# Optimization experiments

Hardware: AMD Instinct MI355X
Metric: run time of the kernel (lower is better)

The kernel has to match this reference:

```python
import jax, jax.numpy as jnp
import numpy as np

N_HEAD = 16
D_MODEL = 1024
D_HEAD = 64
SCALE = 1.0 / D_HEAD ** 0.5
LN_EPS = 1e-5


def layer_norm(x, g, b):
    mu = jnp.mean(x, axis=-1, keepdims=True)
    var = jnp.mean(jnp.square(x - mu), axis=-1, keepdims=True)
    return (x - mu) * jax.lax.rsqrt(var + LN_EPS) * g + b


def setup_inputs() -> dict:
    key = jax.random.key(0)
    ks = jax.random.split(key, 6)
    T, B = 2048, 4
    h = jax.random.normal(ks[0], (T, B, D_MODEL), dtype=jnp.float32)
    # key-padding mask, shape (klen, bsz); True = masked
    attn_mask = jax.random.randint(ks[1], (T, B), 0, 2).astype(jnp.bool_)
    s = 1.0 / np.sqrt(D_MODEL)
    wq = jax.random.uniform(ks[2], (N_HEAD * D_HEAD, D_MODEL), minval=-s, maxval=s, dtype=jnp.float32)
    wkv = jax.random.uniform(ks[3], (2 * N_HEAD * D_HEAD, D_MODEL), minval=-s, maxval=s, dtype=jnp.float32)
    wo = jax.random.uniform(ks[4], (D_MODEL, N_HEAD * D_HEAD), minval=-s, maxval=s, dtype=jnp.float32)
    ln_g = jnp.ones((D_MODEL,), jnp.float32)
    ln_b = jnp.zeros((D_MODEL,), jnp.float32)
    return {"h": h, "attn_mask": attn_mask, "wq": wq, "wkv": wkv,
            "wo": wo, "ln_g": ln_g, "ln_b": ln_b}


def reference(h, attn_mask, wq, wkv, wo, ln_g, ln_b):
    T, B, _ = h.shape
    c = h  # mems is None
    head_q = (h @ wq.T).reshape(T, B, N_HEAD, D_HEAD)
    kv = c @ wkv.T
    head_k, head_v = jnp.split(kv, 2, axis=-1)
    head_k = head_k.reshape(T, B, N_HEAD, D_HEAD)
    head_v = head_v.reshape(T, B, N_HEAD, D_HEAD)

    # scores: [qlen, klen, bsz, n_head]
    attn_score = jnp.einsum('ibnd,jbnd->ijbn', head_q, head_k) * SCALE
    attn_score = jnp.where(attn_mask[None, :, :, None], -jnp.inf, attn_score)
    attn_prob = jax.nn.softmax(attn_score, axis=1)

    attn_vec = jnp.einsum('ijbn,jbnd->ibnd', attn_prob, head_v)
    attn_vec = attn_vec.reshape(T, B, N_HEAD * D_HEAD)
    attn_out = attn_vec @ wo.T
    # post-lnorm residual (pre_lnorm=False); gate='plus' path unused here
    return layer_norm(h + attn_out, ln_g, ln_b)
```

## Files before the change

kernel.cpp:

```cpp
#include <hip/hip_runtime.h>

#define T_LEN 2048
#define BSZ 4
#define NHEAD 16
#define DHEAD 64
#define DMODEL 1024
#define SCALE 0.125f
#define L2E_SCALE (0.125f * 1.44269504f)
#define ROW 72

typedef __bf16 bf16x8 __attribute__((ext_vector_type(8)));
typedef float f32x4 __attribute__((ext_vector_type(4)));

__device__ __forceinline__ float bf2f(unsigned short u) {
  union { unsigned int i; float f; } v; v.i = ((unsigned int)u) << 16; return v.f;
}
__device__ __forceinline__ unsigned short f2bf(float f) {
  union { float f; unsigned int i; } v; v.f = f;
  unsigned int r = v.i + 0x7fffu + ((v.i >> 16) & 1u);
  return (unsigned short)(r >> 16);
}

typedef __attribute__((address_space(1))) void* gptr_t;
typedef __attribute__((address_space(3))) void* lptr_t;

__device__ __forceinline__ void load_lds16(const void* g, void* l) {
  __builtin_amdgcn_global_load_lds((gptr_t)g, (lptr_t)l, 16, 0, 0);
}

__global__ __launch_bounds__(256) void cvt_prep(const float* __restrict__ h,
                                                const float* __restrict__ wq,
                                                const float* __restrict__ wkv,
                                                const float* __restrict__ wo,
                                                const unsigned char* __restrict__ mask,
                                                unsigned short* __restrict__ h_bf,
                                                unsigned short* __restrict__ wq_bf,
                                                unsigned short* __restrict__ wkv_bf,
                                                unsigned short* __restrict__ wo_bf,
                                                int* __restrict__ pos,
                                                int* __restrict__ nkeys) {
  const int tid = threadIdx.x;
  if (blockIdx.x < 12288) {
    const size_t E4 = (size_t)T_LEN * BSZ * DMODEL / 4;
    const size_t W4 = (size_t)NHEAD * DHEAD * DMODEL / 4;
    const size_t g = (size_t)blockIdx.x * 256 + tid;
    const float* src; unsigned short* dst; size_t off;
    if (g < E4)                { src = h;   dst = h_bf;   off = g; }
    else if (g < E4 + W4)      { src = wq;  dst = wq_bf;  off = g - E4; }
    else if (g < E4 + 3 * W4)  { src = wkv; dst = wkv_bf; off = g - E4 - W4; }
    else                       { src = wo;  dst = wo_bf;  off = g - E4 - 3 * W4; }
    const float4 v = *(const float4*)(src + off * 4);
    ushort4 o;
    o.x = f2bf(v.x); o.y = f2bf(v.y); o.z = f2bf(v.z); o.w = f2bf(v.w);
    *(ushort4*)(dst + off * 4) = o;
    return;
  }
  __shared__ int s_any;
  if (tid == 0) s_any = 0;
  __syncthreads();
  int acc = 0;
  for (int i = tid; i < T_LEN * BSZ; i += 256)
    if ((i & 3) != 0 && mask[i] != 0) acc = 1;
  if (acc) atomicOr(&s_any, 1);
  __syncthreads();
  const int mmode = s_any ? 0 : 1;
  const int wv = tid >> 6, lane = tid & 63;
  const int b = wv;
  int run = 0;
  for (int j0 = 0; j0 < T_LEN; j0 += 64) {
    const int j = j0 + lane;
    const int mval = mmode ? ((const int*)mask)[(size_t)j * BSZ + b]
                           : (int)mask[(size_t)j * BSZ + b];
    const int keep = (mval == 0) ? 1 : 0;
    int x = keep;
#pragma unroll
    for (int off = 1; off < 64; off <<= 1) {
      const int y = __shfl_up(x, off, 64);
      if (lane >= off) x += y;
    }
    pos[b * T_LEN + j] = keep ? (run + x - keep) : -1;
    run += __shfl(x, 63, 64);
  }
  if (lane == 0) nkeys[b] = run;
}

#define GEMM64_DBUF(Aptr, Bptr)                                                        \
  const int tid  = threadIdx.x;                                                        \
  const int lane = tid & 63;                                                           \
  const int wv   = tid >> 6;                                                           \
  const int wr = (wv >> 1) * 64;                                                       \
  const int wc = (wv & 1) * 64;                                                        \
  const int mi   = lane & 15;                                                          \
  const int quad = lane >> 4;                                                          \
  f32x4 acc[4][4] = {};                                                                \
  int rowc[4], colc[4];                                                                \
  _Pragma("unroll")                                                                    \
  for (int c = 0; c < 4; c++) {                                                        \
    const int s = c * 256 + tid;                                                       \
    rowc[c] = s >> 3;                                                                  \
    colc[c] = ((s & 7) ^ (rowc[c] & 7)) * 8;                                           \
  }                                                                                    \
  const int swz = mi & 7;                                                              \
  _Pragma("unroll")                                                                    \
  for (int c = 0; c < 4; c++) {                                                        \
    load_lds16(Aptr + (size_t)rowc[c] * DMODEL + colc[c], As + c * 2048 + wv * 512);   \
    load_lds16(Bptr + (size_t)rowc[c] * DMODEL + colc[c], Bs + c * 2048 + wv * 512);   \
  }                                                                                    \
  for (int k0 = 0; k0 < DMODEL; k0 += 64) {                                            \
    const int cur = (k0 >> 6) & 1;                                                     \
    const unsigned short* Asr = As + cur * 8192;                                       \
    const unsigned short* Bsr = Bs + cur * 8192;                                       \
    unsigned short* Asw = As + (1 - cur) * 8192;                                       \
    unsigned short* Bsw = Bs + (1 - cur) * 8192;                                       \
    __syncthreads();                                                                   \
    if (k0 + 64 < DMODEL) {                                                            \
      _Pragma("unroll")                                                                \
      for (int c = 0; c < 4; c++) {                                                    \
        load_lds16(Aptr + (size_t)rowc[c] * DMODEL + k0 + 64 + colc[c], Asw + c * 2048 + wv * 512); \
        load_lds16(Bptr + (size_t)rowc[c] * DMODEL + k0 + 64 + colc[c], Bsw + c * 2048 + wv * 512); \
      }                                                                                \
    }                                                                                  \
    _Pragma("unroll")                                                                  \
    for (int kq = 0; kq < 2; kq++) {                                                   \
      const int cp = ((kq * 4 + quad) ^ swz) * 8;                                      \
      bf16x8 af[4], bfr[4];                                                            \
      _Pragma("unroll")                                                                \
      for (int rt = 0; rt < 4; rt++)                                                   \
        af[rt] = *(const bf16x8*)(Asr + (wr + rt * 16 + mi) * 64 + cp);                \
      _Pragma("unroll")                                                                \
      for (int ct = 0; ct < 4; ct++)                                                   \
        bfr[ct] = *(const bf16x8*)(Bsr + (wc + ct * 16 + mi) * 64 + cp);               \
      _Pragma("unroll")                                                                \
      for (int rt = 0; rt < 4; rt++)                                                   \
        _Pragma("unroll")                                                              \
        for (int ct = 0; ct < 4; ct++)                                                 \
          acc[rt][ct] = __builtin_amdgcn_mfma_f32_16x16x32_bf16(af[rt], bfr[ct], acc[rt][ct], 0, 0, 0); \
    }                                                                                  \
  }

__global__ __launch_bounds__(256) void gemm_qkv(const unsigned short* __restrict__ A,
                                                const unsigned short* __restrict__ Wq,
                                                const unsigned short* __restrict__ Wkv,
                                                const int* __restrict__ pos,
                                                unsigned short* __restrict__ outQ,
                                                unsigned short* __restrict__ outK,
                                                unsigned short* __restrict__ outVt) {
  __shared__ alignas(16) unsigned short As[2 * 128 * 64];
  __shared__ alignas(16) unsigned short Bs[2 * 128 * 64];
  const int m0 = blockIdx.y * 128;
  const int n0 = blockIdx.x * 128;
  const unsigned short* Abase = A + (size_t)m0 * DMODEL;
  const unsigned short* Bbase = (n0 < DMODEL) ? (Wq + (size_t)n0 * DMODEL)
                                              : (Wkv + (size_t)(n0 - DMODEL) * DMODEL);
  GEMM64_DBUF(Abase, Bbase)

  const int region = n0 >> 10;
#pragma unroll
  for (int rt = 0; rt < 4; rt++) {
#pragma unroll
    for (int r = 0; r < 4; r++) {
      const int gm = m0 + wr + rt * 16 + quad * 4 + r;
      const int i = gm >> 2, b = gm & 3;
      int p = i;
      if (region > 0) p = pos[b * T_LEN + i];
      if (region > 0 && p < 0) continue;
#pragma unroll
      for (int ct = 0; ct < 4; ct++) {
        const int gn = n0 + wc + ct * 16 + mi;
        const int gnl = gn & (DMODEL - 1);
        const int hn = gnl >> 6, d = gnl & 63;
        const float v = acc[rt][ct][r];
        if (region == 0)
          outQ[(((size_t)b * NHEAD + hn) * T_LEN + i) * DHEAD + d] = f2bf(v * L2E_SCALE);
        else if (region == 1)
          outK[(((size_t)b * NHEAD + hn) * T_LEN + p) * DHEAD + d] = f2bf(v);
        else
          outVt[(((size_t)b * NHEAD + hn) * DHEAD + d) * T_LEN + p] = f2bf(v);
      }
    }
  }
}

__global__ __launch_bounds__(256) void gemm_out(const unsigned short* __restrict__ A,
                                                const unsigned short* __restrict__ Bw,
                                                unsigned short* __restrict__ outB) {
  __shared__ alignas(16) unsigned short As[2 * 128 * 64];
  __shared__ alignas(16) unsigned short Bs[2 * 128 * 64];
  const int m0 = blockIdx.y * 128;
  const int n0 = blockIdx.x * 128;
  const unsigned short* Abase = A  + (size_t)m0 * DMODEL;
  const unsigned short* Bbase = Bw + (size_t)n0 * DMODEL;
  GEMM64_DBUF(Abase, Bbase)

#pragma unroll
  for (int rt = 0; rt < 4; rt++)
#pragma unroll
    for (int ct = 0; ct < 4; ct++)
#pragma unroll
      for (int r = 0; r < 4; r++) {
        const int gm = m0 + wr + rt * 16 + quad * 4 + r;
        const int gn = n0 + wc + ct * 16 + mi;
        outB[(size_t)gm * DMODEL + gn] = f2bf(acc[rt][ct][r]);
      }
}

template<bool TAIL>
__device__ __forceinline__ void attn_chunk(int j0, int nk, int mi, int quad,
    const unsigned short* Ks, const unsigned short* Vts, unsigned short* PsW,
    const bf16x8 (&qb)[2][2], f32x4 (&oc)[2][4], float (&rs)[2]) {
  f32x4 sc[2][4] = {};
#pragma unroll
  for (int ct = 0; ct < 4; ct++) {
    const bf16x8 kf0 = *(const bf16x8*)(Ks + (ct * 16 + mi) * ROW + quad * 8);
    const bf16x8 kf1 = *(const bf16x8*)(Ks + (ct * 16 + mi) * ROW + 32 + quad * 8);
#pragma unroll
    for (int g = 0; g < 2; g++) {
      sc[g][ct] = __builtin_amdgcn_mfma_f32_16x16x32_bf16(kf0, qb[g][0], sc[g][ct], 0, 0, 0);
      sc[g][ct] = __builtin_amdgcn_mfma_f32_16x16x32_bf16(kf1, qb[g][1], sc[g][ct], 0, 0, 0);
    }
  }
#pragma unroll
  for (int g = 0; g < 2; g++)
#pragma unroll
    for (int ct = 0; ct < 4; ct++) {
#pragma unroll
      for (int r = 0; r < 4; r++) {
        float p = __builtin_amdgcn_exp2f(sc[g][ct][r]);
        if (TAIL && (j0 + ct * 16 + quad * 4 + r >= nk)) p = 0.f;
        rs[g] += p;
        sc[g][ct][r] = p;
      }
      union { float f; unsigned u; } c0, c1, c2, c3;
      c0.f = sc[g][ct][0]; c1.f = sc[g][ct][1]; c2.f = sc[g][ct][2]; c3.f = sc[g][ct][3];
      const unsigned pk0 = (c0.u >> 16) | (c1.u & 0xFFFF0000u);
      const unsigned pk1 = (c2.u >> 16) | (c3.u & 0xFFFF0000u);
      *(uint2*)(PsW + (g * 16 + mi) * ROW + ct * 16 + quad * 4) = make_uint2(pk0, pk1);
    }
  bf16x8 pa0[2], pa1[2];
#pragma unroll
  for (int g = 0; g < 2; g++) {
    pa0[g] = *(const bf16x8*)(PsW + (g * 16 + mi) * ROW + quad * 8);
    pa1[g] = *(const bf16x8*)(PsW + (g * 16 + mi) * ROW + 32 + quad * 8);
  }
#pragma unroll
  for (int ct = 0; ct < 4; ct++) {
    const bf16x8 vf0 = *(const bf16x8*)(Vts + (ct * 16 + mi) * ROW + quad * 8);
    const bf16x8 vf1 = *(const bf16x8*)(Vts + (ct * 16 + mi) * ROW + 32 + quad * 8);
#pragma unroll
    for (int g = 0; g < 2; g++) {
      oc[g][ct] = __builtin_amdgcn_mfma_f32_16x16x32_bf16(pa0[g], vf0, oc[g][ct], 0, 0, 0);
      oc[g][ct] = __builtin_amdgcn_mfma_f32_16x16x32_bf16(pa1[g], vf1, oc[g][ct], 0, 0, 0);
    }
  }
}

__global__ __launch_bounds__(256, 4) void attn_mfma(const unsigned short* __restrict__ Qg,
                                                    const unsigned short* __restrict__ Kg,
                                                    const unsigned short* __restrict__ Vtg,
                                                    const int* __restrict__ nkeys,
                                                    unsigned short* __restrict__ av) {
  __shared__ alignas(16) unsigned short smem[18688];
  unsigned short* Ks  = smem;
  unsigned short* Vts = smem + 4608;
  unsigned short* Qs  = smem + 9216;
  float* Ls = (float*)(smem + 18432);

  const int tid  = threadIdx.x;
  const int lane = tid & 63;
  const int wv   = tid >> 6;
  const int mi   = lane & 15;
  const int quad = lane >> 4;
  const int i0 = blockIdx.x * 128;
  const int b  = blockIdx.y;
  const int n  = blockIdx.z;
  const size_t base = ((size_t)b * NHEAD + n) * T_LEN * DHEAD;
  const int nk = nkeys[b];

  for (int it = tid; it < 1024; it += 256) {
    const int r = it >> 3, c8 = (it & 7) * 8;
    *(uint4*)(Qs + r * ROW + c8) = *(const uint4*)(Qg + base + (size_t)(i0 + r) * DHEAD + c8);
  }
  __syncthreads();
  bf16x8 qb[2][2];
#pragma unroll
  for (int g = 0; g < 2; g++) {
    qb[g][0] = *(const bf16x8*)(Qs + (wv * 32 + g * 16 + mi) * ROW + quad * 8);
    qb[g][1] = *(const bf16x8*)(Qs + (wv * 32 + g * 16 + mi) * ROW + 32 + quad * 8);
  }

  f32x4 oc[2][4] = {};
  float rs[2] = {0.f, 0.f};
  unsigned short* PsW = Qs + wv * 2304;

  const int nmain = nk & ~63;
  for (int j0 = 0; j0 < nmain; j0 += 64) {
    for (int it = tid; it < 512; it += 256) {
      const int r = it >> 3, c8 = (it & 7) * 8;
      *(uint4*)(Ks  + r * ROW + c8) = *(const uint4*)(Kg  + base + (size_t)(j0 + r) * DHEAD + c8);
      *(uint4*)(Vts + r * ROW + c8) = *(const uint4*)(Vtg + base + (size_t)r * T_LEN + j0 + c8);
    }
    __syncthreads();
    attn_chunk<false>(j0, nk, mi, quad, Ks, Vts, PsW, qb, oc, rs);
    __syncthreads();
  }
  if (nmain < nk) {
    for (int it = tid; it < 512; it += 256) {
      const int r = it >> 3, c8 = (it & 7) * 8;
      *(uint4*)(Ks  + r * ROW + c8) = *(const uint4*)(Kg  + base + (size_t)(nmain + r) * DHEAD + c8);
      *(uint4*)(Vts + r * ROW + c8) = *(const uint4*)(Vtg + base + (size_t)r * T_LEN + nmain + c8);
    }
    __syncthreads();
    attn_chunk<true>(nmain, nk, mi, quad, Ks, Vts, PsW, qb, oc, rs);
  }

#pragma unroll
  for (int g = 0; g < 2; g++) {
    float t = rs[g];
    t += __shfl_xor(t, 16, 64);
    t += __shfl_xor(t, 32, 64);
    rs[g] = t;
  }
  if (quad == 0) { Ls[wv * 32 + mi] = rs[0]; Ls[wv * 32 + 16 + mi] = rs[1]; }
  __syncthreads();
  float linv[2][4];
#pragma unroll
  for (int g = 0; g < 2; g++)
#pragma unroll
    for (int r = 0; r < 4; r++) {
      const float l = Ls[wv * 32 + g * 16 + quad * 4 + r];
      linv[g][r] = (l > 0.f) ? (1.f / l) : 0.f;
    }
#pragma unroll
  for (int g = 0; g < 2; g++)
#pragma unroll
    for (int ct = 0; ct < 4; ct++)
#pragma unroll
      for (int r = 0; r < 4; r++) {
        const int q = i0 + wv * 32 + g * 16 + quad * 4 + r;
        const int d = ct * 16 + mi;
        av[((size_t)q * BSZ + b) * DMODEL + n * DHEAD + d] = f2bf(oc[g][ct][r] * linv[g][r]);
      }
}

__global__ __launch_bounds__(256) void ln_kernel(const float* __restrict__ h,
                                                 const unsigned short* __restrict__ ao,
                                                 const float* __restrict__ g,
                                                 const float* __restrict__ bb,
                                                 float* __restrict__ out) {
  __shared__ float red[16];
  const int row = blockIdx.x;
  const int tid = threadIdx.x;
  const size_t base = (size_t)row * DMODEL;
  const int c = tid * 4;
  const float4 hv = *(const float4*)(h + base + c);
  const ushort4 a4 = *(const ushort4*)(ao + base + c);
  float x[4] = { hv.x + bf2f(a4.x), hv.y + bf2f(a4.y), hv.z + bf2f(a4.z), hv.w + bf2f(a4.w) };
  float s = 0.f, sq = 0.f;
#pragma unroll
  for (int k = 0; k < 4; k++) { s += x[k]; sq += x[k] * x[k]; }
#pragma unroll
  for (int off = 32; off; off >>= 1) { s += __shfl_xor(s, off, 64); sq += __shfl_xor(sq, off, 64); }
  const int wv = tid >> 6, lane = tid & 63;
  if (lane == 0) { red[wv] = s; red[8 + wv] = sq; }
  __syncthreads();
  if (tid == 0) {
    float ts = 0.f, tq = 0.f;
    for (int w = 0; w < 4; w++) { ts += red[w]; tq += red[8 + w]; }
    red[4] = ts; red[12] = tq;
  }
  __syncthreads();
  const float mu  = red[4] * (1.f / DMODEL);
  const float var = red[12] * (1.f / DMODEL) - mu * mu;
  const float inv = rsqrtf(var + 1e-5f);
  const float4 gv = *(const float4*)(g + c);
  const float4 bv = *(const float4*)(bb + c);
  float4 o;
  o.x = (x[0] - mu) * inv * gv.x + bv.x;
  o.y = (x[1] - mu) * inv * gv.y + bv.y;
  o.z = (x[2] - mu) * inv * gv.z + bv.z;
  o.w = (x[3] - mu) * inv * gv.w + bv.w;
  *(float4*)(out + base + c) = o;
}

extern "C" void kernel_launch(void* const* d_in, const int* in_sizes, int n_in,
                              void* d_out, int out_size, void* d_ws, size_t ws_size,
                              hipStream_t stream) {
  (void)in_sizes; (void)n_in; (void)out_size; (void)ws_size;
  const float* h           = (const float*)d_in[0];
  const unsigned char* msk = (const unsigned char*)d_in[1];
  const float* wq          = (const float*)d_in[2];
  const float* wkv         = (const float*)d_in[3];
  const float* wo          = (const float*)d_in[4];
  const float* lng         = (const float*)d_in[5];
  const float* lnb         = (const float*)d_in[6];
  float* out = (float*)d_out;

  const size_t E  = (size_t)T_LEN * BSZ * DMODEL;
  const size_t WQ = (size_t)NHEAD * DHEAD * DMODEL;
  char* ws = (char*)d_ws;
  int* nkeys            = (int*)ws;                       ws += 16;
  int* pos              = (int*)ws;                       ws += (size_t)BSZ * T_LEN * 4;
  unsigned short* h_bf  = (unsigned short*)ws;            ws += E * 2;
  unsigned short* wq_bf = (unsigned short*)ws;            ws += WQ * 2;
  unsigned short* wkv_bf= (unsigned short*)ws;            ws += 2 * WQ * 2;
  unsigned short* wo_bf = (unsigned short*)ws;            ws += WQ * 2;
  unsigned short* Qb    = (unsigned short*)ws;            ws += E * 2;
  unsigned short* Kb    = (unsigned short*)ws;            ws += E * 2;
  unsigned short* Vtb   = (unsigned short*)ws;            ws += E * 2;
  unsigned short* AV    = (unsigned short*)ws;            ws += E * 2;
  unsigned short* AO    = (unsigned short*)ws;

  const dim3 blk(256);
  cvt_prep<<<dim3(12289), blk, 0, stream>>>(h, wq, wkv, wo, msk,
                                            h_bf, wq_bf, wkv_bf, wo_bf, pos, nkeys);
  gemm_qkv<<<dim3(3 * DMODEL / 128, T_LEN * BSZ / 128), blk, 0, stream>>>(
      h_bf, wq_bf, wkv_bf, pos, Qb, Kb, Vtb);
  attn_mfma<<<dim3(T_LEN / 128, BSZ, NHEAD), blk, 0, stream>>>(Qb, Kb, Vtb, nkeys, AV);
  gemm_out<<<dim3(DMODEL / 128, T_LEN * BSZ / 128), blk, 0, stream>>>(AV, wo_bf, AO);
  ln_kernel<<<dim3(T_LEN * BSZ), blk, 0, stream>>>(h, AO, lng, lnb, out);
}
```

Before: 312.7 us.

## Rewrite QKV and output GEMMs with larger tiles and a 4-stage LDS ring

```diff
diff --git a/kernel.cpp b/kernel.cpp
--- a/kernel.cpp
+++ b/kernel.cpp
@@ -84,92 +84,133 @@
   if (lane == 0) nkeys[b] = run;
 }
 
-#define GEMM64_DBUF(Aptr, Bptr)                                                        \
-  const int tid  = threadIdx.x;                                                        \
-  const int lane = tid & 63;                                                           \
-  const int wv   = tid >> 6;                                                           \
-  const int wr = (wv >> 1) * 64;                                                       \
-  const int wc = (wv & 1) * 64;                                                        \
-  const int mi   = lane & 15;                                                          \
-  const int quad = lane >> 4;                                                          \
-  f32x4 acc[4][4] = {};                                                                \
-  int rowc[4], colc[4];                                                                \
-  _Pragma("unroll")                                                                    \
-  for (int c = 0; c < 4; c++) {                                                        \
-    const int s = c * 256 + tid;                                                       \
-    rowc[c] = s >> 3;                                                                  \
-    colc[c] = ((s & 7) ^ (rowc[c] & 7)) * 8;                                           \
-  }                                                                                    \
-  const int swz = mi & 7;                                                              \
-  _Pragma("unroll")                                                                    \
-  for (int c = 0; c < 4; c++) {                                                        \
-    load_lds16(Aptr + (size_t)rowc[c] * DMODEL + colc[c], As + c * 2048 + wv * 512);   \
-    load_lds16(Bptr + (size_t)rowc[c] * DMODEL + colc[c], Bs + c * 2048 + wv * 512);   \
-  }                                                                                    \
-  for (int k0 = 0; k0 < DMODEL; k0 += 64) {                                            \
-    const int cur = (k0 >> 6) & 1;                                                     \
-    const unsigned short* Asr = As + cur * 8192;                                       \
-    const unsigned short* Bsr = Bs + cur * 8192;                                       \
-    unsigned short* Asw = As + (1 - cur) * 8192;                                       \
-    unsigned short* Bsw = Bs + (1 - cur) * 8192;                                       \
-    __syncthreads();                                                                   \
-    if (k0 + 64 < DMODEL) {                                                            \
-      _Pragma("unroll")                                                                \
-      for (int c = 0; c < 4; c++) {                                                    \
-        load_lds16(Aptr + (size_t)rowc[c] * DMODEL + k0 + 64 + colc[c], Asw + c * 2048 + wv * 512); \
-        load_lds16(Bptr + (size_t)rowc[c] * DMODEL + k0 + 64 + colc[c], Bsw + c * 2048 + wv * 512); \
-      }                                                                                \
-    }                                                                                  \
-    _Pragma("unroll")                                                                  \
-    for (int kq = 0; kq < 2; kq++) {                                                   \
-      const int cp = ((kq * 4 + quad) ^ swz) * 8;                                      \
-      bf16x8 af[4], bfr[4];                                                            \
-      _Pragma("unroll")                                                                \
-      for (int rt = 0; rt < 4; rt++)                                                   \
-        af[rt] = *(const bf16x8*)(Asr + (wr + rt * 16 + mi) * 64 + cp);                \
-      _Pragma("unroll")                                                                \
-      for (int ct = 0; ct < 4; ct++)                                                   \
-        bfr[ct] = *(const bf16x8*)(Bsr + (wc + ct * 16 + mi) * 64 + cp);               \
-      _Pragma("unroll")                                                                \
-      for (int rt = 0; rt < 4; rt++)                                                   \
-        _Pragma("unroll")                                                              \
-        for (int ct = 0; ct < 4; ct++)                                                 \
-          acc[rt][ct] = __builtin_amdgcn_mfma_f32_16x16x32_bf16(af[rt], bfr[ct], acc[rt][ct], 0, 0, 0); \
-    }                                                                                  \
-  }
-
-__global__ __launch_bounds__(256) void gemm_qkv(const unsigned short* __restrict__ A,
-                                                const unsigned short* __restrict__ Wq,
-                                                const unsigned short* __restrict__ Wkv,
-                                                const int* __restrict__ pos,
-                                                unsigned short* __restrict__ outQ,
-                                                unsigned short* __restrict__ outK,
-                                                unsigned short* __restrict__ outVt) {
-  __shared__ alignas(16) unsigned short As[2 * 128 * 64];
-  __shared__ alignas(16) unsigned short Bs[2 * 128 * 64];
-  const int m0 = blockIdx.y * 128;
-  const int n0 = blockIdx.x * 128;
+
+__device__ __forceinline__ bf16x8 ldfrag(const unsigned short* slot, int row, int quad) {
+  return *(const bf16x8*)(slot + row * 32 + (((quad ^ (row >> 1)) & 3) * 8));
+}
+
+template<int C>
+__device__ __forceinline__ void stage32(const unsigned short* gsrc,
+                                        unsigned short* slot, int tid) {
+#pragma unroll
+  for (int c = 0; c < C; ++c) {
+    const int g = c * 512 + tid;
+    const int row = g >> 2;
+    const int lc = (g ^ (row >> 1)) & 3;
+    load_lds16(gsrc + (size_t)row * DMODEL + lc * 8,
+               slot + c * 4096 + (tid >> 6) * 512);
+  }
+}
+
+template<int N>
+__device__ __forceinline__ void wait_vm() {
+  if constexpr (N == 0)      asm volatile("s_waitcnt vmcnt(0)" ::: "memory");
+  else if constexpr (N == 3) asm volatile("s_waitcnt vmcnt(3)" ::: "memory");
+  else if constexpr (N == 4) asm volatile("s_waitcnt vmcnt(4)" ::: "memory");
+  else if constexpr (N == 6) asm volatile("s_waitcnt vmcnt(6)" ::: "memory");
+  else                       asm volatile("s_waitcnt vmcnt(8)" ::: "memory");
+}
+
+template<int MF, int NF, int BRA, int BRB>
+__device__ __forceinline__ void gemm_ring(const unsigned short* __restrict__ Abase,
+                                          const unsigned short* __restrict__ Bbase,
+                                          unsigned short* As, unsigned short* Bs,
+                                          f32x4 (&acc)[MF][NF],
+                                          int tid, int mi, int quad, int wrow, int wcol) {
+  constexpr int LA = BRA / 128, LB = BRB / 128;
+  constexpr int SA = BRA * 32, SB = BRB * 32;
+  constexpr int PH = MF / 4;
+  constexpr int NKT = DMODEL / 32;
+  constexpr int INF = (LA + LB) * 2;
+
+#pragma unroll
+  for (int p = 0; p < 3; ++p) {
+    stage32<LA>(Abase + p * 32, As + p * SA, tid);
+    stage32<LB>(Bbase + p * 32, Bs + p * SB, tid);
+  }
+
+  for (int kt = 0; kt < NKT; ++kt) {
+    const unsigned short* Asl = As + (kt & 3) * SA;
+    const unsigned short* Bsl = Bs + (kt & 3) * SB;
+    unsigned short* Asw = As + ((kt + 3) & 3) * SA;
+    unsigned short* Bsw = Bs + ((kt + 3) & 3) * SB;
+    if (kt < NKT - 2)       wait_vm<INF>();
+    else if (kt == NKT - 2) wait_vm<INF / 2>();
+    else                    wait_vm<0>();
+    __builtin_amdgcn_s_barrier();
+    const bool pre = (kt + 3 < NKT);
+    bf16x8 bfr[NF];
+#pragma unroll
+    for (int ph = 0; ph < PH; ++ph) {
+      if (ph == 0) {
+#pragma unroll
+        for (int nf = 0; nf < NF; ++nf)
+          bfr[nf] = ldfrag(Bsl, wcol + nf * 16 + mi, quad);
+      }
+      bf16x8 af[4];
+#pragma unroll
+      for (int m = 0; m < 4; ++m)
+        af[m] = ldfrag(Asl, wrow + (ph * 4 + m) * 16 + mi, quad);
+      if (pre) {
+        if (ph == 0)      stage32<LA>(Abase + (kt + 3) * 32, Asw, tid);
+        if (ph == PH - 1) stage32<LB>(Bbase + (kt + 3) * 32, Bsw, tid);
+      }
+      __builtin_amdgcn_s_barrier();
+      asm volatile("s_waitcnt lgkmcnt(0)" ::: "memory");
+      __builtin_amdgcn_sched_barrier(0);
+      __builtin_amdgcn_s_setprio(1);
+#pragma unroll
+      for (int m = 0; m < 4; ++m)
+#pragma unroll
+        for (int nf = 0; nf < NF; ++nf)
+          acc[ph * 4 + m][nf] = __builtin_amdgcn_mfma_f32_16x16x32_bf16(
+              af[m], bfr[nf], acc[ph * 4 + m][nf], 0, 0, 0);
+      __builtin_amdgcn_s_setprio(0);
+      __builtin_amdgcn_s_barrier();
+    }
+  }
+}
+
+__global__ __launch_bounds__(512, 2) void gemm_qkv(const unsigned short* __restrict__ A,
+                                                   const unsigned short* __restrict__ Wq,
+                                                   const unsigned short* __restrict__ Wkv,
+                                                   const int* __restrict__ pos,
+                                                   unsigned short* __restrict__ outQ,
+                                                   unsigned short* __restrict__ outK,
+                                                   unsigned short* __restrict__ outVt) {
+  __shared__ alignas(16) unsigned short As[4 * 256 * 32];
+  __shared__ alignas(16) unsigned short Bs[4 * 256 * 32];
+  const int tid  = threadIdx.x;
+  const int lane = tid & 63;
+  const int wv   = tid >> 6;
+  const int mi   = lane & 15;
+  const int quad = lane >> 4;
+  const int wrow = (wv >> 2) * 128;
+  const int wcol = (wv & 3) * 64;
+  const int m0 = blockIdx.y * 256;
+  const int n0 = blockIdx.x * 256;
   const unsigned short* Abase = A + (size_t)m0 * DMODEL;
   const unsigned short* Bbase = (n0 < DMODEL) ? (Wq + (size_t)n0 * DMODEL)
                                               : (Wkv + (size_t)(n0 - DMODEL) * DMODEL);
-  GEMM64_DBUF(Abase, Bbase)
+  f32x4 acc[8][4] = {};
+  gemm_ring<8, 4, 256, 256>(Abase, Bbase, As, Bs, acc, tid, mi, quad, wrow, wcol);
 
   const int region = n0 >> 10;
 #pragma unroll
-  for (int rt = 0; rt < 4; rt++) {
+  for (int mf = 0; mf < 8; mf++) {
 #pragma unroll
     for (int r = 0; r < 4; r++) {
-      const int gm = m0 + wr + rt * 16 + quad * 4 + r;
+      const int gm = m0 + wrow + mf * 16 + quad * 4 + r;
       const int i = gm >> 2, b = gm & 3;
       int p = i;
       if (region > 0) p = pos[b * T_LEN + i];
       if (region > 0 && p < 0) continue;
 #pragma unroll
-      for (int ct = 0; ct < 4; ct++) {
-        const int gn = n0 + wc + ct * 16 + mi;
+      for (int nf = 0; nf < 4; nf++) {
+        const int gn = n0 + wcol + nf * 16 + mi;
         const int gnl = gn & (DMODEL - 1);
         const int hn = gnl >> 6, d = gnl & 63;
-        const float v = acc[rt][ct][r];
+        const float v = acc[mf][nf][r];
         if (region == 0)
           outQ[(((size_t)b * NHEAD + hn) * T_LEN + i) * DHEAD + d] = f2bf(v * L2E_SCALE);
         else if (region == 1)
@@ -181,26 +222,34 @@
   }
 }
 
-__global__ __launch_bounds__(256) void gemm_out(const unsigned short* __restrict__ A,
-                                                const unsigned short* __restrict__ Bw,
-                                                unsigned short* __restrict__ outB) {
-  __shared__ alignas(16) unsigned short As[2 * 128 * 64];
-  __shared__ alignas(16) unsigned short Bs[2 * 128 * 64];
-  const int m0 = blockIdx.y * 128;
+__global__ __launch_bounds__(512, 2) void gemm_out(const unsigned short* __restrict__ A,
+                                                   const unsigned short* __restrict__ Bw,
+                                                   unsigned short* __restrict__ outB) {
+  __shared__ alignas(16) unsigned short As[4 * 256 * 32];
+  __shared__ alignas(16) unsigned short Bs[4 * 128 * 32];
+  const int tid  = threadIdx.x;
+  const int lane = tid & 63;
+  const int wv   = tid >> 6;
+  const int mi   = lane & 15;
+  const int quad = lane >> 4;
+  const int wrow = (wv >> 1) * 64;
+  const int wcol = (wv & 1) * 64;
+  const int m0 = blockIdx.y * 256;
   const int n0 = blockIdx.x * 128;
   const unsigned short* Abase = A  + (size_t)m0 * DMODEL;
   const unsigned short* Bbase = Bw + (size_t)n0 * DMODEL;
-  GEMM64_DBUF(Abase, Bbase)
-
-#pragma unroll
-  for (int rt = 0; rt < 4; rt++)
-#pragma unroll
-    for (int ct = 0; ct < 4; ct++)
+  f32x4 acc[4][4] = {};
+  gemm_ring<4, 4, 256, 128>(Abase, Bbase, As, Bs, acc, tid, mi, quad, wrow, wcol);
+
+#pragma unroll
+  for (int mf = 0; mf < 4; mf++)
+#pragma unroll
+    for (int nf = 0; nf < 4; nf++)
 #pragma unroll
       for (int r = 0; r < 4; r++) {
-        const int gm = m0 + wr + rt * 16 + quad * 4 + r;
-        const int gn = n0 + wc + ct * 16 + mi;
-        outB[(size_t)gm * DMODEL + gn] = f2bf(acc[rt][ct][r]);
+        const int gm = m0 + wrow + mf * 16 + quad * 4 + r;
+        const int gn = n0 + wcol + nf * 16 + mi;
+        outB[(size_t)gm * DMODEL + gn] = f2bf(acc[mf][nf][r]);
       }
 }
 
@@ -410,12 +459,11 @@
   unsigned short* AV    = (unsigned short*)ws;            ws += E * 2;
   unsigned short* AO    = (unsigned short*)ws;
 
-  const dim3 blk(256);
-  cvt_prep<<<dim3(12289), blk, 0, stream>>>(h, wq, wkv, wo, msk,
-                                            h_bf, wq_bf, wkv_bf, wo_bf, pos, nkeys);
-  gemm_qkv<<<dim3(3 * DMODEL / 128, T_LEN * BSZ / 128), blk, 0, stream>>>(
+  cvt_prep<<<dim3(12289), dim3(256), 0, stream>>>(h, wq, wkv, wo, msk,
+                                                  h_bf, wq_bf, wkv_bf, wo_bf, pos, nkeys);
+  gemm_qkv<<<dim3(3 * DMODEL / 256, T_LEN * BSZ / 256), dim3(512), 0, stream>>>(
       h_bf, wq_bf, wkv_bf, pos, Qb, Kb, Vtb);
-  attn_mfma<<<dim3(T_LEN / 128, BSZ, NHEAD), blk, 0, stream>>>(Qb, Kb, Vtb, nkeys, AV);
-  gemm_out<<<dim3(DMODEL / 128, T_LEN * BSZ / 128), blk, 0, stream>>>(AV, wo_bf, AO);
-  ln_kernel<<<dim3(T_LEN * BSZ), blk, 0, stream>>>(h, AO, lng, lnb, out);
-}
+  attn_mfma<<<dim3(T_LEN / 128, BSZ, NHEAD), dim3(256), 0, stream>>>(Qb, Kb, Vtb, nkeys, AV);
+  gemm_out<<<dim3(DMODEL / 128, T_LEN * BSZ / 256), dim3(512), 0, stream>>>(AV, wo_bf, AO);
+  ln_kernel<<<dim3(T_LEN * BSZ), dim3(256), 0, stream>>>(h, AO, lng, lnb, out);
+}
```

Measured after the change: 328.6 us. +5.1%, slower.

## Prefetch next K/V chunk into registers while computing current attention chunk

Applied to the files above, without the earlier changes.

```diff
diff --git a/kernel.cpp b/kernel.cpp
--- a/kernel.cpp
+++ b/kernel.cpp
@@ -254,7 +254,7 @@
   }
 }
 
-__global__ __launch_bounds__(256, 4) void attn_mfma(const unsigned short* __restrict__ Qg,
+__global__ __launch_bounds__(256, 3) void attn_mfma(const unsigned short* __restrict__ Qg,
                                                     const unsigned short* __restrict__ Kg,
                                                     const unsigned short* __restrict__ Vtg,
                                                     const int* __restrict__ nkeys,
@@ -292,26 +292,43 @@
   float rs[2] = {0.f, 0.f};
   unsigned short* PsW = Qs + wv * 2304;
 
-  const int nmain = nk & ~63;
-  for (int j0 = 0; j0 < nmain; j0 += 64) {
-    for (int it = tid; it < 512; it += 256) {
-      const int r = it >> 3, c8 = (it & 7) * 8;
-      *(uint4*)(Ks  + r * ROW + c8) = *(const uint4*)(Kg  + base + (size_t)(j0 + r) * DHEAD + c8);
-      *(uint4*)(Vts + r * ROW + c8) = *(const uint4*)(Vtg + base + (size_t)r * T_LEN + j0 + c8);
-    }
+  const int sr  = tid >> 3;
+  const int sc8 = (tid & 7) * 8;
+  uint4 kreg0, kreg1, vreg0, vreg1;
+
+#define ATTN_ISSUE(J0)                                                                   \
+  kreg0 = *(const uint4*)(Kg  + base + (size_t)((J0) + sr) * DHEAD + sc8);               \
+  kreg1 = *(const uint4*)(Kg  + base + (size_t)((J0) + sr + 32) * DHEAD + sc8);          \
+  vreg0 = *(const uint4*)(Vtg + base + (size_t)sr * T_LEN + (J0) + sc8);                 \
+  vreg1 = *(const uint4*)(Vtg + base + (size_t)(sr + 32) * T_LEN + (J0) + sc8);
+
+#define ATTN_COMMIT()                                                                    \
+  *(uint4*)(Ks  + sr * ROW + sc8)        = kreg0;                                        \
+  *(uint4*)(Ks  + (sr + 32) * ROW + sc8) = kreg1;                                        \
+  *(uint4*)(Vts + sr * ROW + sc8)        = vreg0;                                        \
+  *(uint4*)(Vts + (sr + 32) * ROW + sc8) = vreg1;
+
+  const int nc = (nk + 63) >> 6;
+  if (nc > 0) {
+    ATTN_ISSUE(0)
+    ATTN_COMMIT()
     __syncthreads();
-    attn_chunk<false>(j0, nk, mi, quad, Ks, Vts, PsW, qb, oc, rs);
-    __syncthreads();
-  }
-  if (nmain < nk) {
-    for (int it = tid; it < 512; it += 256) {
-      const int r = it >> 3, c8 = (it & 7) * 8;
-      *(uint4*)(Ks  + r * ROW + c8) = *(const uint4*)(Kg  + base + (size_t)(nmain + r) * DHEAD + c8);
-      *(uint4*)(Vts + r * ROW + c8) = *(const uint4*)(Vtg + base + (size_t)r * T_LEN + nmain + c8);
-    }
-    __syncthreads();
-    attn_chunk<true>(nmain, nk, mi, quad, Ks, Vts, PsW, qb, oc, rs);
-  }
+    for (int c = 0; c < nc; ++c) {
+      const int j0 = c * 64;
+      if (c + 1 < nc) { ATTN_ISSUE(j0 + 64) }
+      if (c == nc - 1 && (nk & 63))
+        attn_chunk<true>(j0, nk, mi, quad, Ks, Vts, PsW, qb, oc, rs);
+      else
+        attn_chunk<false>(j0, nk, mi, quad, Ks, Vts, PsW, qb, oc, rs);
+      __syncthreads();
+      if (c + 1 < nc) {
+        ATTN_COMMIT()
+        __syncthreads();
+      }
+    }
+  }
+#undef ATTN_ISSUE
+#undef ATTN_COMMIT
 
 #pragma unroll
   for (int g = 0; g < 2; g++) {
```

New measurement: 323.3 us. +3.4%, slower.
